# Performance work log

Hardware: AMD Instinct MI355X
Metric: run time of the kernel (lower is better)

## Reference

```python
import jax, jax.numpy as jnp
import numpy as np

EPS = 1e-5


def _conv1x1(h, w, b):
    # 1x1 conv == per-pixel matmul: (b,c,h,w) x (o,c) -> (b,o,h,w)
    return jnp.einsum('bchw,oc->bohw', h, w) + b[None, :, None, None]


def setup_inputs() -> dict:
    key = jax.random.key(0)
    ks = jax.random.split(key, 7)
    B, C, H, W = 4, 512, 64, 64
    s = 0.02
    return {
        'x': jax.random.normal(ks[0], (B, C, H, W), dtype=jnp.float32),
        'wq': jax.random.normal(ks[1], (C, C), dtype=jnp.float32) * s,
        'bq': jax.random.normal(ks[2], (C,), dtype=jnp.float32) * s,
        'wk': jax.random.normal(ks[3], (C, C), dtype=jnp.float32) * s,
        'bk': jax.random.normal(ks[4], (C,), dtype=jnp.float32) * s,
        'wv': jax.random.normal(ks[5], (C, C), dtype=jnp.float32) * s,
        'bv': jax.random.normal(ks[6], (C,), dtype=jnp.float32) * s,
    }


def reference(x, wq, bq, wk, bk, wv, bv):
    B, C, H, W = x.shape
    # InstanceNorm2d (affine=False): normalize over spatial dims per (b, c)
    mu = jnp.mean(x, axis=(2, 3), keepdims=True)
    var = jnp.var(x, axis=(2, 3), keepdims=True)  # biased, matches torch
    h_ = (x - mu) * jax.lax.rsqrt(var + EPS)

    q = _conv1x1(h_, wq, bq).reshape(B, C, H * W)  # (b, c, n)
    k = _conv1x1(h_, wk, bk).reshape(B, C, H * W)
    v = _conv1x1(h_, wv, bv).reshape(B, C, H * W)

    scale = float(int(C)) ** (-0.5)
    attn = jnp.einsum('bcq,bck->bqk', q, k) * scale  # (b, n_q, n_k)
    attn = jax.nn.softmax(attn, axis=-1)
    # torch: bmm(v, attn.permute(0,2,1)) -> A[b,c,q] = sum_k v[b,c,k] * attn[b,q,k]
    A = jnp.einsum('bck,bqk->bcq', v, attn).reshape(B, C, H, W)
    return x + A
```

## Files before the change

### kernel.cpp

```cpp
#include <hip/hip_runtime.h>
#include <hip/hip_bf16.h>
#include <cstdint>

#define B_ 4
#define C_ 512
#define N_ 4096

typedef unsigned short u16;
typedef unsigned char u8;
typedef __bf16 bf16x8 __attribute__((ext_vector_type(8)));
typedef float f32x4 __attribute__((ext_vector_type(4)));

union U16B { uint4 u; bf16x8 v; };

__device__ __forceinline__ bf16x8 ld16g(const u16* p) {
  U16B t; t.u = *(const uint4*)p; return t.v;
}

__device__ __forceinline__ u16 f2bf(float f) {
  uint32_t u = __builtin_bit_cast(uint32_t, f);
  u = (u + 0x7FFFu + ((u >> 16) & 1u)) >> 16;
  return (u16)u;
}
__device__ __forceinline__ float bf2f(u16 h) {
  uint32_t u = ((uint32_t)h) << 16;
  return __builtin_bit_cast(float, u);
}

__device__ __forceinline__ u8 f2fp8(float f) {
  uint32_t u = __builtin_bit_cast(uint32_t, f);
  uint32_t s = (u >> 24) & 0x80u;
  uint32_t a = u & 0x7FFFFFFFu;
  if (a >= 0x43700000u) return (u8)(s | 0x7E);
  if (a < 0x3C800000u) {
    float af = __builtin_bit_cast(float, a);
    int m = (int)(af * 512.0f + 0.5f);
    return (u8)(s | (uint32_t)m);
  }
  uint32_t r = (a + 0x7FFFFu + ((a >> 20) & 1u)) >> 20;
  return (u8)(s | (r - (120u << 3)));
}

typedef const __attribute__((address_space(1))) uint32_t* gas_p;
typedef __attribute__((address_space(3))) uint32_t* las_p;
__device__ __forceinline__ void gld16(const void* g, void* l) {
  __builtin_amdgcn_global_load_lds((gas_p)g, (las_p)l, 16, 0, 0);
}

#define SCEXP 0.06376149809794171f

__global__ __launch_bounds__(256) void cvt_w(const float* __restrict__ w, u16* __restrict__ o) {
  int i = blockIdx.x * 256 + threadIdx.x;
  float4 v = ((const float4*)w)[i];
  ushort4 r;
  r.x = f2bf(v.x); r.y = f2bf(v.y); r.z = f2bf(v.z); r.w = f2bf(v.w);
  ((ushort4*)o)[i] = r;
}

__global__ __launch_bounds__(1024) void pack_bias(const float* __restrict__ bq,
    const float* __restrict__ bk, float* __restrict__ o) {
  int i = threadIdx.x;
  o[i] = (i < 512) ? bq[i] : bk[i - 512];
}

__global__ __launch_bounds__(256) void inorm_stats(const float* __restrict__ x,
    float* __restrict__ mu, float* __restrict__ rstd) {
  int bc = blockIdx.x;
  const float4* p = (const float4*)(x + (size_t)bc * N_);
  float s = 0.f, ss = 0.f;
  for (int i = threadIdx.x; i < N_ / 4; i += 256) {
    float4 v = p[i];
    s  += v.x + v.y + v.z + v.w;
    ss += v.x * v.x + v.y * v.y + v.z * v.z + v.w * v.w;
  }
#pragma unroll
  for (int off = 32; off > 0; off >>= 1) {
    s  += __shfl_down(s, off);
    ss += __shfl_down(ss, off);
  }
  __shared__ float as_[4], ass_[4];
  if ((threadIdx.x & 63) == 0) { as_[threadIdx.x >> 6] = s; ass_[threadIdx.x >> 6] = ss; }
  __syncthreads();
  if (threadIdx.x == 0) {
    float S  = as_[0] + as_[1] + as_[2] + as_[3];
    float SS = ass_[0] + ass_[1] + ass_[2] + ass_[3];
    float m  = S * (1.f / N_);
    float var = SS * (1.f / N_) - m * m;
    mu[bc] = m;
    rstd[bc] = rsqrtf(var + 1e-5f);
  }
}

__global__ __launch_bounds__(256) void norm_transpose(const float* __restrict__ x,
    const float* __restrict__ mu, const float* __restrict__ rstd, u16* __restrict__ hT) {
  __shared__ u16 tile[64][66];
  int b = blockIdx.z, c0 = blockIdx.y * 64, n0 = blockIdx.x * 64;
  int tn = threadIdx.x & 63, t4 = threadIdx.x >> 6;
  const float* xb = x + ((size_t)b * C_ + c0) * N_ + n0;
#pragma unroll
  for (int it = 0; it < 16; ++it) {
    int c = t4 + it * 4;
    float m  = mu[b * C_ + c0 + c];
    float rs = rstd[b * C_ + c0 + c];
    tile[c][tn] = f2bf((xb[(size_t)c * N_ + tn] - m) * rs);
  }
  __syncthreads();
  u16* hTb = hT + ((size_t)b * N_ + n0) * C_ + c0;
#pragma unroll
  for (int it = 0; it < 16; ++it) {
    int n = t4 + it * 4;
    hTb[(size_t)n * C_ + tn] = tile[tn][n];
  }
}

#define EPI_QK8  2
#define EPI_V8   3

template<int EPI>
__global__ __launch_bounds__(256) void gemm128(
    const u16* __restrict__ A, const u16* __restrict__ B,
    const float* __restrict__ aux, void* __restrict__ Out,
    int klen, int lda, int ldb, int ldo,
    long sAz, long sBz, long sOz)
{
  int z = blockIdx.z;
  const u16* Ab = A + (size_t)z * sAz;
  const u16* Bb = B + (size_t)z * sBz;
  int m0 = blockIdx.x * 128, n0 = blockIdx.y * 128;
  int t = threadIdx.x, w = t >> 6, l = t & 63;
  int wr = w >> 1, wc = w & 1;
  int l16 = l & 15, lg = l >> 4;

  __shared__ char smem[65536];

  int srow = t >> 3;
  int scol = ((t & 7) << 4) ^ ((srow & 7) << 4);
  size_t ldaB = (size_t)lda * 2, ldbB = (size_t)ldb * 2;

  f32x4 acc[4][4] = {};
  int nsteps = klen >> 6;

#define STAGE(step, d) {                                                     \
    size_t kbyte = (size_t)(step) * 128 + scol;                              \
    char* lb = smem + (d) * 32768;                                           \
    _Pragma("unroll")                                                        \
    for (int i = 0; i < 4; ++i) {                                            \
      int row = i * 32 + srow;                                               \
      gld16((const char*)Ab + (size_t)(m0 + row) * ldaB + kbyte,             \
            lb + (size_t)(i * 256 + t) * 16);                                \
      gld16((const char*)Bb + (size_t)(n0 + row) * ldbB + kbyte,             \
            lb + 16384 + (size_t)(i * 256 + t) * 16);                        \
    }                                                                        \
  }

  STAGE(0, 0);
  __syncthreads();
  int cur = 0;
  int sw = (l16 & 7) << 4;
  for (int s = 0; s < nsteps; ++s) {
    if (s + 1 < nsteps) STAGE(s + 1, cur ^ 1);
    const char* Al = smem + cur * 32768;
    const char* Bl = Al + 16384;
#pragma unroll
    for (int kc = 0; kc < 2; ++kc) {
      int cb = (kc * 64 + lg * 16) ^ sw;
      bf16x8 af[4], bf[4];
#pragma unroll
      for (int mf = 0; mf < 4; ++mf)
        af[mf] = *(const bf16x8*)(Al + (wr * 64 + mf * 16 + l16) * 128 + cb);
#pragma unroll
      for (int nf = 0; nf < 4; ++nf)
        bf[nf] = *(const bf16x8*)(Bl + (wc * 64 + nf * 16 + l16) * 128 + cb);
#pragma unroll
      for (int mf = 0; mf < 4; ++mf)
#pragma unroll
        for (int nf = 0; nf < 4; ++nf)
          acc[mf][nf] = __builtin_amdgcn_mfma_f32_16x16x32_bf16(af[mf], bf[nf], acc[mf][nf], 0, 0, 0);
    }
    __syncthreads();
    cur ^= 1;
  }
#undef STAGE

  u8* ob = (u8*)Out + (size_t)z * sOz;
  char* sb = smem;
  float bc[4];
  if constexpr (EPI == EPI_QK8) {
#pragma unroll
    for (int nf = 0; nf < 4; ++nf) bc[nf] = aux[n0 + wc * 64 + nf * 16 + l16];
  }
#pragma unroll
  for (int mf = 0; mf < 4; ++mf) {
#pragma unroll
    for (int r = 0; r < 4; ++r) {
      int rowl = wr * 64 + mf * 16 + lg * 4 + r;
      float brow = (EPI == EPI_V8) ? aux[m0 + rowl] : 0.f;
#pragma unroll
      for (int nf = 0; nf < 4; ++nf) {
        int cl = wc * 64 + nf * 16 + l16;
        int w6 = cl & 63;
        int clp = (cl & 64) | (((w6 >> 3) & 3) * 16) | (((w6 >> 5) & 1) * 8) | (w6 & 7);
        float v = acc[mf][nf][r] + (EPI == EPI_QK8 ? bc[nf] : brow);
        sb[rowl * 128 + clp] = (char)f2fp8(v);
      }
    }
  }
  __syncthreads();
#pragma unroll
  for (int it = 0; it < 4; ++it) {
    int idx = it * 256 + t;
    int row = idx >> 3, seg = idx & 7;
    *(uint4*)(ob + (size_t)(m0 + row) * ldo + n0 + seg * 16) =
        *(const uint4*)(sb + row * 128 + seg * 16);
  }
}

__global__ __launch_bounds__(512, 2) void exp8(
    const u8* __restrict__ qk8, float* __restrict__ dsumAll, u8* __restrict__ Pall)
{
  int fid = blockIdx.x;
  int rid = (fid & 7) * 256 + (fid >> 3);
  int z = rid >> 9;
  int r9 = rid & 511;
  int c2 = r9 >> 8;
  int r8 = r9 & 255;
  int sm = r8 >> 6, w6s = r8 & 63;
  int m0 = (c2 * 16 + (sm >> 1) * 8 + (w6s >> 3)) * 128;
  int n0 = ((sm & 1) * 8 + (w6s & 7)) * 256;

  const u8* Ab = qk8 + (size_t)z * ((size_t)N_ * 1024);
  const u8* Bb = Ab + 512;
  float* dsum = dsumAll + (size_t)z * N_;
  u8* Pp = Pall + (size_t)z * (size_t)N_ * N_;

  int t = threadIdx.x, w = t >> 6, l = t & 63;
  int wr = w >> 2, wc = w & 3;
  int l16 = l & 15, lg = l >> 4;

  __shared__ char smem[49152];

  f32x4 acc[4][4] = {};
  int rg = ((lg ^ ((l16 >> 1) & 3)) & 3) << 4;

#define STG8(step, lb) {                                                     \
    size_t kb = (size_t)(step) * 64;                                         \
    {                                                                        \
      int row = t >> 2, g = t & 3;                                           \
      int sg = (g ^ ((row >> 1) & 3)) << 4;                                  \
      gld16((const char*)Ab + (size_t)(m0 + row) * 1024 + kb + sg,           \
            (lb) + (size_t)t * 16);                                          \
    }                                                                        \
    _Pragma("unroll")                                                        \
    for (int i = 0; i < 2; ++i) {                                            \
      int s2 = i * 512 + t;                                                  \
      int row = s2 >> 2, g = s2 & 3;                                         \
      int sg = (g ^ ((row >> 1) & 3)) << 4;                                  \
      gld16((const char*)Bb + (size_t)(n0 + row) * 1024 + kb + sg,           \
            (lb) + 8192 + (size_t)s2 * 16);                                  \
    }                                                                        \
  }

#define COMP8(lb) {                                                          \
    const char* Al = (lb);                                                   \
    const char* Bl = (lb) + 8192;                                            \
    uint4 af[4], bf[4];                                                      \
    _Pragma("unroll")                                                        \
    for (int mf = 0; mf < 4; ++mf)                                           \
      af[mf] = *(const uint4*)(Al + (wr * 64 + mf * 16 + l16) * 64 + rg);    \
    _Pragma("unroll")                                                        \
    for (int nf = 0; nf < 4; ++nf)                                           \
      bf[nf] = *(const uint4*)(Bl + (wc * 64 + nf * 16 + l16) * 64 + rg);    \
    _Pragma("unroll")                                                        \
    for (int kk = 0; kk < 2; ++kk) {                                         \
      _Pragma("unroll")                                                      \
      for (int mf = 0; mf < 4; ++mf) {                                       \
        long long a8 = ((long long)(kk ? af[mf].w : af[mf].y) << 32) |       \
                       (unsigned int)(kk ? af[mf].z : af[mf].x);             \
        _Pragma("unroll")                                                    \
        for (int nf = 0; nf < 4; ++nf) {                                     \
          long long b8 = ((long long)(kk ? bf[nf].w : bf[nf].y) << 32) |     \
                         (unsigned int)(kk ? bf[nf].z : bf[nf].x);           \
          acc[mf][nf] = __builtin_amdgcn_mfma_f32_16x16x32_fp8_fp8(          \
              a8, b8, acc[mf][nf], 0, 0, 0);                                 \
        }                                                                    \
      }                                                                      \
    }                                                                        \
  }

  char* buf0 = smem;
  char* buf1 = smem + 24576;

  STG8(0, buf0);
#pragma unroll
  for (int s = 0; s < 8; ++s) {
    char* cb = (s & 1) ? buf1 : buf0;
    char* nb = (s & 1) ? buf0 : buf1;
    if (s < 7) {
      STG8(s + 1, nb);
      asm volatile("s_waitcnt vmcnt(3)" ::: "memory");
    } else {
      asm volatile("s_waitcnt vmcnt(0)" ::: "memory");
    }
    __builtin_amdgcn_s_barrier();
    __builtin_amdgcn_sched_barrier(0);
    COMP8(cb);
    __builtin_amdgcn_sched_barrier(0);
    __builtin_amdgcn_s_barrier();
  }
#undef STG8
#undef COMP8

#pragma unroll
  for (int mf = 0; mf < 4; ++mf) {
#pragma unroll
    for (int r = 0; r < 4; ++r) {
      int row = wr * 64 + mf * 16 + lg * 4 + r;
      float rs = 0.f;
#pragma unroll
      for (int nf = 0; nf < 4; ++nf) {
        int cl = wc * 64 + nf * 16 + l16;
        int w6 = cl & 63;
        int clp = (cl & 192) | (((w6 >> 3) & 3) * 16) | (((w6 >> 5) & 1) * 8) | (w6 & 7);
        float p = __builtin_amdgcn_exp2f(acc[mf][nf][r] * SCEXP);
        rs += p;
        smem[row * 256 + clp] = (char)f2fp8(p);
      }
      rs += __shfl_xor(rs, 1); rs += __shfl_xor(rs, 2);
      rs += __shfl_xor(rs, 4); rs += __shfl_xor(rs, 8);
      if (l16 == 0) atomicAdd(&dsum[m0 + row], rs);
    }
  }
  __syncthreads();
#pragma unroll
  for (int it = 0; it < 4; ++it) {
    int idx = it * 512 + t;
    int row = idx >> 4, seg = idx & 15;
    *(uint4*)(Pp + ((size_t)(m0 + row) * N_ + n0 + seg * 16)) =
        *(const uint4*)(smem + row * 256 + seg * 16);
  }
}

__global__ __launch_bounds__(256, 4) void pv8(
    const u8* __restrict__ vM8, const u8* __restrict__ P8,
    const float* __restrict__ denom, const float* __restrict__ x,
    float* __restrict__ out)
{
  int fid = blockIdx.x;
  int rid = (fid & 7) * 64 + (fid >> 3);
  int z = rid >> 7;
  int r7 = rid & 127;
  int n0 = (r7 >> 2) * 128;
  int m0 = (r7 & 3) * 128;

  const u8* Ab = vM8 + (size_t)z * ((size_t)C_ * N_);
  const u8* Bb = P8 + (size_t)z * ((size_t)N_ * N_);
  const float* db = denom + (size_t)z * N_;
  const float* xb = x + (size_t)z * ((size_t)C_ * N_);
  float* ob = out + (size_t)z * ((size_t)C_ * N_);

  int t = threadIdx.x, w = t >> 6, l = t & 63;
  int wr = w >> 1, wc = w & 1;
  int l16 = l & 15, lg = l >> 4;

  __shared__ char smem[32768];

  f32x4 acc[4][4] = {};
  int rg = ((lg ^ ((l16 >> 1) & 3)) & 3) << 4;

#define STGP(step, lb) {                                                     \
    size_t kb = (size_t)(step) * 64;                                         \
    _Pragma("unroll")                                                        \
    for (int i = 0; i < 2; ++i) {                                            \
      int s2 = i * 256 + t;                                                  \
      int row = s2 >> 2, g = s2 & 3;                                         \
      int sg = (g ^ ((row >> 1) & 3)) << 4;                                  \
      gld16((const char*)Ab + (size_t)(m0 + row) * N_ + kb + sg,             \
            (lb) + (size_t)s2 * 16);                                         \
      gld16((const char*)Bb + (size_t)(n0 + row) * N_ + kb + sg,             \
            (lb) + 8192 + (size_t)s2 * 16);                                  \
    }                                                                        \
  }

#define COMPP(lb) {                                                          \
    const char* Al = (lb);                                                   \
    const char* Bl = (lb) + 8192;                                            \
    uint4 af[4], bf[4];                                                      \
    _Pragma("unroll")                                                        \
    for (int mf = 0; mf < 4; ++mf)                                           \
      af[mf] = *(const uint4*)(Al + (wr * 64 + mf * 16 + l16) * 64 + rg);    \
    _Pragma("unroll")                                                        \
    for (int nf = 0; nf < 4; ++nf)                                           \
      bf[nf] = *(const uint4*)(Bl + (wc * 64 + nf * 16 + l16) * 64 + rg);    \
    _Pragma("unroll")                                                        \
    for (int kk = 0; kk < 2; ++kk) {                                         \
      _Pragma("unroll")                                                      \
      for (int mf = 0; mf < 4; ++mf) {                                       \
        long long a8 = ((long long)(kk ? af[mf].w : af[mf].y) << 32) |       \
                       (unsigned int)(kk ? af[mf].z : af[mf].x);             \
        _Pragma("unroll")                                                    \
        for (int nf = 0; nf < 4; ++nf) {                                     \
          long long b8 = ((long long)(kk ? bf[nf].w : bf[nf].y) << 32) |     \
                         (unsigned int)(kk ? bf[nf].z : bf[nf].x);           \
          acc[mf][nf] = __builtin_amdgcn_mfma_f32_16x16x32_fp8_fp8(          \
              a8, b8, acc[mf][nf], 0, 0, 0);                                 \
        }                                                                    \
      }                                                                      \
    }                                                                        \
  }

  char* buf0 = smem;
  char* buf1 = smem + 16384;

  STGP(0, buf0);
#pragma unroll 2
  for (int s = 0; s < 64; ++s) {
    char* cb = (s & 1) ? buf1 : buf0;
    char* nb = (s & 1) ? buf0 : buf1;
    if (s < 63) {
      STGP(s + 1, nb);
      asm volatile("s_waitcnt vmcnt(4)" ::: "memory");
    } else {
      asm volatile("s_waitcnt vmcnt(0)" ::: "memory");
    }
    __builtin_amdgcn_s_barrier();
    __builtin_amdgcn_sched_barrier(0);
    COMPP(cb);
    __builtin_amdgcn_sched_barrier(0);
    __builtin_amdgcn_s_barrier();
  }
#undef STGP
#undef COMPP

  float rd[4];
#pragma unroll
  for (int nf = 0; nf < 4; ++nf)
    rd[nf] = 1.0f / db[n0 + wc * 64 + nf * 16 + l16];
#pragma unroll
  for (int mf = 0; mf < 4; ++mf) {
#pragma unroll
    for (int r = 0; r < 4; ++r) {
      int row = m0 + wr * 64 + mf * 16 + lg * 4 + r;
#pragma unroll
      for (int nf = 0; nf < 4; ++nf) {
        int col = n0 + wc * 64 + nf * 16 + l16;
        size_t o = (size_t)row * N_ + col;
        ob[o] = xb[o] + acc[mf][nf][r] * rd[nf];
      }
    }
  }
}

__global__ __launch_bounds__(256) void gemm_abT(
    const u16* __restrict__ A, const u16* __restrict__ Bm,
    const float* __restrict__ bias, u16* __restrict__ out,
    int ldo, int bias_is_row)
{
  int w = threadIdx.x >> 6, l = threadIdx.x & 63;
  int l16 = l & 15, lg = l >> 4;
  int m0 = blockIdx.x * 128 + (w >> 1) * 64;
  int n0 = blockIdx.y * 128 + (w & 1) * 64;
  f32x4 acc[4][4] = {};
  const u16* Ab = A  + (size_t)(m0 + l16) * 512 + lg * 8;
  const u16* Bb = Bm + (size_t)(n0 + l16) * 512 + lg * 8;
  for (int kc = 0; kc < 512; kc += 32) {
    bf16x8 af[4], bf[4];
#pragma unroll
    for (int i = 0; i < 4; ++i) af[i] = ld16g(Ab + (size_t)(i * 16) * 512 + kc);
#pragma unroll
    for (int j = 0; j < 4; ++j) bf[j] = ld16g(Bb + (size_t)(j * 16) * 512 + kc);
#pragma unroll
    for (int i = 0; i < 4; ++i)
#pragma unroll
      for (int j = 0; j < 4; ++j)
        acc[i][j] = __builtin_amdgcn_mfma_f32_16x16x32_bf16(af[i], bf[j], acc[i][j], 0, 0, 0);
  }
#pragma unroll
  for (int i = 0; i < 4; ++i) {
#pragma unroll
    for (int j = 0; j < 4; ++j) {
      int col = n0 + j * 16 + l16;
#pragma unroll
      for (int r = 0; r < 4; ++r) {
        int row = m0 + i * 16 + lg * 4 + r;
        float v = acc[i][j][r] + (bias_is_row ? bias[row] : bias[col]);
        out[(size_t)row * ldo + col] = f2bf(v);
      }
    }
  }
}

#define NQ 32
#define NKB 64
__global__ __launch_bounds__(512) void attn_kernel(
    const u16* __restrict__ qT, const u16* __restrict__ kT, const u16* __restrict__ vM,
    const float* __restrict__ x, float* __restrict__ out)
{
  int b = blockIdx.y;
  int nq0 = blockIdx.x * NQ;
  const u16* qTb = qT + (size_t)b * N_ * C_;
  const u16* kTb = kT + (size_t)b * N_ * C_;
  const u16* vb  = vM + (size_t)b * C_ * N_;
  const float* xb = x + (size_t)b * C_ * N_;
  float* ob = out + (size_t)b * C_ * N_;

  int tid = threadIdx.x;
  int w = tid >> 6, l = tid & 63, l16 = l & 15, lg = l >> 4;
  int nqf = w & 1, nkf = w >> 1;
  int c0 = w * 64;

  __shared__ u16 qlds[32][520];
  __shared__ u16 Plds[32][72];
  __shared__ float dpart[32][16];
  __shared__ float dfin[32];

  for (int idx = tid; idx < 32 * 64; idx += 512) {
    int row = idx >> 6, cg = idx & 63;
    *(uint4*)&qlds[row][cg * 8] = *(const uint4*)(qTb + (size_t)(nq0 + row) * C_ + cg * 8);
  }
  __syncthreads();

  f32x4 acc[2][4] = {};
  float dreg = 0.f;
  int drow = tid >> 4, dcol = (tid & 15) * 4;

  for (int nk0 = 0; nk0 < N_; nk0 += NKB) {
    f32x4 s = {0.f, 0.f, 0.f, 0.f};
    const u16* krow = kTb + (size_t)(nk0 + nkf * 16 + l16) * C_ + lg * 8;
#pragma unroll 4
    for (int kc = 0; kc < 16; ++kc) {
      U16B tq; tq.u = *(const uint4*)&qlds[nqf * 16 + l16][kc * 32 + lg * 8];
      bf16x8 kf = ld16g(krow + kc * 32);
      s = __builtin_amdgcn_mfma_f32_16x16x32_bf16(tq.v, kf, s, 0, 0, 0);
    }
    __syncthreads();
#pragma unroll
    for (int r = 0; r < 4; ++r) {
      float p = __builtin_amdgcn_exp2f(s[r] * SCEXP);
      Plds[nqf * 16 + lg * 4 + r][nkf * 16 + l16] = f2bf(p);
    }
    __syncthreads();
#pragma unroll
    for (int r = 0; r < 4; ++r) dreg += bf2f(Plds[drow][dcol + r]);
#pragma unroll
    for (int kk = 0; kk < 2; ++kk) {
      bf16x8 pf[2];
#pragma unroll
      for (int i = 0; i < 2; ++i) {
        U16B t2; t2.u = *(const uint4*)&Plds[i * 16 + l16][kk * 32 + lg * 8];
        pf[i] = t2.v;
      }
#pragma unroll
      for (int j = 0; j < 4; ++j) {
        bf16x8 vf = ld16g(vb + (size_t)(c0 + j * 16 + l16) * N_ + nk0 + kk * 32 + lg * 8);
#pragma unroll
        for (int i = 0; i < 2; ++i)
          acc[i][j] = __builtin_amdgcn_mfma_f32_16x16x32_bf16(pf[i], vf, acc[i][j], 0, 0, 0);
      }
    }
  }

  dpart[drow][tid & 15] = dreg;
  __syncthreads();
  if (tid < 32) {
    float s2 = 0.f;
#pragma unroll
    for (int g = 0; g < 16; ++g) s2 += dpart[tid][g];
    dfin[tid] = s2;
  }
  __syncthreads();

#pragma unroll
  for (int i = 0; i < 2; ++i) {
    float dinv[4];
#pragma unroll
    for (int r = 0; r < 4; ++r) dinv[r] = 1.f / dfin[i * 16 + lg * 4 + r];
    int nbase = nq0 + i * 16 + lg * 4;
#pragma unroll
    for (int j = 0; j < 4; ++j) {
      int c = c0 + j * 16 + l16;
      float4 xv = *(const float4*)(xb + (size_t)c * N_ + nbase);
      float4 o;
      o.x = xv.x + acc[i][j][0] * dinv[0];
      o.y = xv.y + acc[i][j][1] * dinv[1];
      o.z = xv.z + acc[i][j][2] * dinv[2];
      o.w = xv.w + acc[i][j][3] * dinv[3];
      *(float4*)(ob + (size_t)c * N_ + nbase) = o;
    }
  }
}

extern "C" void kernel_launch(void* const* d_in, const int* in_sizes, int n_in,
                              void* d_out, int out_size, void* d_ws, size_t ws_size,
                              hipStream_t stream) {
  (void)in_sizes; (void)n_in; (void)out_size;
  const float* x  = (const float*)d_in[0];
  const float* wq = (const float*)d_in[1];
  const float* bq = (const float*)d_in[2];
  const float* wk = (const float*)d_in[3];
  const float* bk = (const float*)d_in[4];
  const float* wv = (const float*)d_in[5];
  const float* bv = (const float*)d_in[6];
  float* out = (float*)d_out;
  char* ws = (char*)d_ws;

  const size_t NC = (size_t)N_ * C_;
  const size_t NEED = 136380416;

  if (ws_size >= NEED) {
    u16*   wbf_q = (u16*)(ws);
    u16*   wbf_k = (u16*)(ws + 524288);
    u16*   wbf_v = (u16*)(ws + 1048576);
    float* bqk   = (float*)(ws + 1572864);
    float* mu    = (float*)(ws + 1581056);
    float* rstd  = (float*)(ws + 1589248);
    u16*   hT    = (u16*)(ws + 1597440);
    u8*    qk8   = (u8*)(ws + 18874368);
    u8*    vM8   = (u8*)(ws + 52428800);
    float* denom = (float*)(ws + 69206016);
    u8*    P8    = (u8*)(ws + 69271552);

    cvt_w<<<256, 256, 0, stream>>>(wq, wbf_q);
    cvt_w<<<256, 256, 0, stream>>>(wk, wbf_k);
    cvt_w<<<256, 256, 0, stream>>>(wv, wbf_v);
    pack_bias<<<1, 1024, 0, stream>>>(bq, bk, bqk);
    inorm_stats<<<B_ * C_, 256, 0, stream>>>(x, mu, rstd);
    norm_transpose<<<dim3(N_ / 64, C_ / 64, B_), 256, 0, stream>>>(x, mu, rstd, hT);
    hipMemsetAsync(denom, 0, 4 * N_ * sizeof(float), stream);

    gemm128<EPI_QK8><<<dim3(32, 8, 4), 256, 0, stream>>>(
        hT, wbf_q, bqk, qk8, 512, 512, 512, 1024, (long)NC, 0, (long)N_ * 1024);
    gemm128<EPI_V8><<<dim3(4, 32, 4), 256, 0, stream>>>(
        wbf_v, hT, bv, vM8, 512, 512, 512, 4096, 0, (long)NC, (long)NC);

    exp8<<<2048, 512, 0, stream>>>(qk8, denom, P8);

    pv8<<<512, 256, 0, stream>>>(vM8, P8, denom, x, out);
  } else {
    u16*   wbf_q = (u16*)(ws);
    u16*   wbf_k = (u16*)(ws + 524288);
    u16*   wbf_v = (u16*)(ws + 1048576);
    float* mu    = (float*)(ws + 1572864);
    float* rstd  = (float*)(ws + 1581056);
    u16*   hT    = (u16*)(ws + 1589248);
    u16*   qT    = (u16*)(ws + 18366464);
    u16*   kT    = (u16*)(ws + 35143680);
    u16*   vM    = (u16*)(ws + 51920896);

    cvt_w<<<256, 256, 0, stream>>>(wq, wbf_q);
    cvt_w<<<256, 256, 0, stream>>>(wk, wbf_k);
    cvt_w<<<256, 256, 0, stream>>>(wv, wbf_v);
    inorm_stats<<<B_ * C_, 256, 0, stream>>>(x, mu, rstd);
    norm_transpose<<<dim3(N_ / 64, C_ / 64, B_), 256, 0, stream>>>(x, mu, rstd, hT);

    for (int b = 0; b < B_; ++b) {
      const u16* hTb = hT + (size_t)b * NC;
      u16* qTb = qT + (size_t)b * NC;
      u16* kTb = kT + (size_t)b * NC;
      u16* vMb = vM + (size_t)b * NC;
      gemm_abT<<<dim3(N_ / 128, C_ / 128), 256, 0, stream>>>(hTb, wbf_q, bq, qTb, C_, 0);
      gemm_abT<<<dim3(N_ / 128, C_ / 128), 256, 0, stream>>>(hTb, wbf_k, bk, kTb, C_, 0);
      gemm_abT<<<dim3(C_ / 128, N_ / 128), 256, 0, stream>>>(wbf_v, hTb, bv, vMb, N_, 1);
    }
    attn_kernel<<<dim3(N_ / NQ, B_), 512, 0, stream>>>(qT, kT, vM, x, out);
  }
}
```

Before: 227.7 us.

## Split exp kernel into single-wave 64x64 tiles and store probabilities as bf8

Replaces the 512-thread, 128x256-tile exp kernel with a one-wavefront kernel over 64x64 tiles. It uses a triple-buffered global-to-LDS pipeline with no block barriers and launches 16384 blocks. Probabilities are now encoded as bf8 (e5m2) through a half-precision conversion rather than fp8, and the PV kernel switches to fp8*bf8 MFMA with 8-byte LDS fragment loads. The column permutation in the epilogue stores is dropped. Smaller tiles re-read the Q/K operands more often, and bf8 carries less mantissa precision for the softmax weights.

```diff
diff --git a/kernel.cpp b/kernel.cpp
--- a/kernel.cpp
+++ b/kernel.cpp
@@ -39,6 +39,13 @@
   }
   uint32_t r = (a + 0x7FFFFu + ((a >> 20) & 1u)) >> 20;
   return (u8)(s | (r - (120u << 3)));
+}
+
+__device__ __forceinline__ u8 f2bf8pos(float f) {
+  _Float16 h = (_Float16)f;
+  u16 hb = __builtin_bit_cast(unsigned short, h);
+  hb = (u16)(hb + 0x7Fu + ((hb >> 8) & 1u));
+  return (u8)(hb >> 8);
 }
 
 typedef const __attribute__((address_space(1))) uint32_t* gas_p;
@@ -198,10 +205,8 @@
 #pragma unroll
       for (int nf = 0; nf < 4; ++nf) {
         int cl = wc * 64 + nf * 16 + l16;
-        int w6 = cl & 63;
-        int clp = (cl & 64) | (((w6 >> 3) & 3) * 16) | (((w6 >> 5) & 1) * 8) | (w6 & 7);
         float v = acc[mf][nf][r] + (EPI == EPI_QK8 ? bc[nf] : brow);
-        sb[rowl * 128 + clp] = (char)f2fp8(v);
+        sb[rowl * 128 + cl] = (char)f2fp8(v);
       }
     }
   }
@@ -215,128 +220,106 @@
   }
 }
 
-__global__ __launch_bounds__(512, 2) void exp8(
+__global__ __launch_bounds__(64, 2) void exp_wave(
     const u8* __restrict__ qk8, float* __restrict__ dsumAll, u8* __restrict__ Pall)
 {
   int fid = blockIdx.x;
-  int rid = (fid & 7) * 256 + (fid >> 3);
-  int z = rid >> 9;
-  int r9 = rid & 511;
-  int c2 = r9 >> 8;
-  int r8 = r9 & 255;
-  int sm = r8 >> 6, w6s = r8 & 63;
-  int m0 = (c2 * 16 + (sm >> 1) * 8 + (w6s >> 3)) * 128;
-  int n0 = ((sm & 1) * 8 + (w6s & 7)) * 256;
+  int rid = (fid & 7) * 2048 + (fid >> 3);
+  int z = rid >> 12;
+  int r12 = rid & 4095;
+  int st = r12 >> 6, w6 = r12 & 63;
+  int m0 = ((st >> 3) * 8 + (w6 >> 3)) * 64;
+  int n0 = ((st & 7) * 8 + (w6 & 7)) * 64;
 
   const u8* Ab = qk8 + (size_t)z * ((size_t)N_ * 1024);
   const u8* Bb = Ab + 512;
   float* dsum = dsumAll + (size_t)z * N_;
   u8* Pp = Pall + (size_t)z * (size_t)N_ * N_;
 
-  int t = threadIdx.x, w = t >> 6, l = t & 63;
-  int wr = w >> 2, wc = w & 3;
-  int l16 = l & 15, lg = l >> 4;
-
-  __shared__ char smem[49152];
+  int l = threadIdx.x, l16 = l & 15, lg = l >> 4;
+
+  __shared__ char smem[12288];
 
   f32x4 acc[4][4] = {};
-  int rg = ((lg ^ ((l16 >> 1) & 3)) & 3) << 4;
-
-#define STG8(step, lb) {                                                     \
-    size_t kb = (size_t)(step) * 64;                                         \
-    {                                                                        \
-      int row = t >> 2, g = t & 3;                                           \
-      int sg = (g ^ ((row >> 1) & 3)) << 4;                                  \
-      gld16((const char*)Ab + (size_t)(m0 + row) * 1024 + kb + sg,           \
-            (lb) + (size_t)t * 16);                                          \
+  int ga = ((((lg >> 1) ^ ((l16 >> 2) & 1)) << 4) | ((lg & 1) << 3));
+
+#define STGE(s, lb) {                                                        \
+    size_t kb = (size_t)(s) * 32;                                            \
+    _Pragma("unroll")                                                        \
+    for (int i = 0; i < 2; ++i) {                                            \
+      int slot = i * 64 + l;                                                 \
+      int row = slot >> 1;                                                   \
+      int gs = ((slot & 1) ^ ((row >> 2) & 1)) << 4;                         \
+      gld16((const char*)Ab + (size_t)(m0 + row) * 1024 + kb + gs,           \
+            (lb) + slot * 16);                                               \
+      gld16((const char*)Bb + (size_t)(n0 + row) * 1024 + kb + gs,           \
+            (lb) + 2048 + slot * 16);                                        \
     }                                                                        \
-    _Pragma("unroll")                                                        \
-    for (int i = 0; i < 2; ++i) {                                            \
-      int s2 = i * 512 + t;                                                  \
-      int row = s2 >> 2, g = s2 & 3;                                         \
-      int sg = (g ^ ((row >> 1) & 3)) << 4;                                  \
-      gld16((const char*)Bb + (size_t)(n0 + row) * 1024 + kb + sg,           \
-            (lb) + 8192 + (size_t)s2 * 16);                                  \
-    }                                                                        \
-  }
-
-#define COMP8(lb) {                                                          \
-    const char* Al = (lb);                                                   \
-    const char* Bl = (lb) + 8192;                                            \
-    uint4 af[4], bf[4];                                                      \
+  }
+
+#define COMPE(lb) {                                                          \
+    long long a8[4], b8[4];                                                  \
     _Pragma("unroll")                                                        \
     for (int mf = 0; mf < 4; ++mf)                                           \
-      af[mf] = *(const uint4*)(Al + (wr * 64 + mf * 16 + l16) * 64 + rg);    \
+      a8[mf] = *(const long long*)((lb) + (mf * 16 + l16) * 32 + ga);        \
     _Pragma("unroll")                                                        \
     for (int nf = 0; nf < 4; ++nf)                                           \
-      bf[nf] = *(const uint4*)(Bl + (wc * 64 + nf * 16 + l16) * 64 + rg);    \
-    _Pragma("unroll")                                                        \
-    for (int kk = 0; kk < 2; ++kk) {                                         \
+      b8[nf] = *(const long long*)((lb) + 2048 + (nf * 16 + l16) * 32 + ga); \
+    _Pragma("unroll")                                                        \
+    for (int mf = 0; mf < 4; ++mf)                                           \
       _Pragma("unroll")                                                      \
-      for (int mf = 0; mf < 4; ++mf) {                                       \
-        long long a8 = ((long long)(kk ? af[mf].w : af[mf].y) << 32) |       \
-                       (unsigned int)(kk ? af[mf].z : af[mf].x);             \
-        _Pragma("unroll")                                                    \
-        for (int nf = 0; nf < 4; ++nf) {                                     \
-          long long b8 = ((long long)(kk ? bf[nf].w : bf[nf].y) << 32) |     \
-                         (unsigned int)(kk ? bf[nf].z : bf[nf].x);           \
-          acc[mf][nf] = __builtin_amdgcn_mfma_f32_16x16x32_fp8_fp8(          \
-              a8, b8, acc[mf][nf], 0, 0, 0);                                 \
-        }                                                                    \
-      }                                                                      \
-    }                                                                        \
-  }
-
-  char* buf0 = smem;
-  char* buf1 = smem + 24576;
-
-  STG8(0, buf0);
-#pragma unroll
-  for (int s = 0; s < 8; ++s) {
-    char* cb = (s & 1) ? buf1 : buf0;
-    char* nb = (s & 1) ? buf0 : buf1;
-    if (s < 7) {
-      STG8(s + 1, nb);
-      asm volatile("s_waitcnt vmcnt(3)" ::: "memory");
-    } else {
-      asm volatile("s_waitcnt vmcnt(0)" ::: "memory");
-    }
-    __builtin_amdgcn_s_barrier();
+      for (int nf = 0; nf < 4; ++nf)                                         \
+        acc[mf][nf] = __builtin_amdgcn_mfma_f32_16x16x32_fp8_fp8(            \
+            a8[mf], b8[nf], acc[mf][nf], 0, 0, 0);                           \
+  }
+
+  char* b0 = smem;
+  char* b1 = smem + 4096;
+  char* b2 = smem + 8192;
+
+  STGE(0, b0);
+  STGE(1, b1);
+#pragma unroll
+  for (int s = 0; s < 14; ++s) {
+    STGE(s + 2, b2);
+    asm volatile("s_waitcnt vmcnt(8)" ::: "memory");
     __builtin_amdgcn_sched_barrier(0);
-    COMP8(cb);
-    __builtin_amdgcn_sched_barrier(0);
-    __builtin_amdgcn_s_barrier();
-  }
-#undef STG8
-#undef COMP8
+    COMPE(b0);
+    char* tmp = b0; b0 = b1; b1 = b2; b2 = tmp;
+  }
+  asm volatile("s_waitcnt vmcnt(4)" ::: "memory");
+  __builtin_amdgcn_sched_barrier(0);
+  COMPE(b0);
+  { char* tmp = b0; b0 = b1; b1 = b2; b2 = tmp; }
+  asm volatile("s_waitcnt vmcnt(0)" ::: "memory");
+  __builtin_amdgcn_sched_barrier(0);
+  COMPE(b0);
+#undef STGE
+#undef COMPE
 
 #pragma unroll
   for (int mf = 0; mf < 4; ++mf) {
 #pragma unroll
     for (int r = 0; r < 4; ++r) {
-      int row = wr * 64 + mf * 16 + lg * 4 + r;
+      int row = mf * 16 + lg * 4 + r;
       float rs = 0.f;
 #pragma unroll
       for (int nf = 0; nf < 4; ++nf) {
-        int cl = wc * 64 + nf * 16 + l16;
-        int w6 = cl & 63;
-        int clp = (cl & 192) | (((w6 >> 3) & 3) * 16) | (((w6 >> 5) & 1) * 8) | (w6 & 7);
         float p = __builtin_amdgcn_exp2f(acc[mf][nf][r] * SCEXP);
         rs += p;
-        smem[row * 256 + clp] = (char)f2fp8(p);
+        smem[row * 64 + nf * 16 + l16] = (char)f2bf8pos(p);
       }
       rs += __shfl_xor(rs, 1); rs += __shfl_xor(rs, 2);
       rs += __shfl_xor(rs, 4); rs += __shfl_xor(rs, 8);
       if (l16 == 0) atomicAdd(&dsum[m0 + row], rs);
     }
   }
-  __syncthreads();
 #pragma unroll
   for (int it = 0; it < 4; ++it) {
-    int idx = it * 512 + t;
-    int row = idx >> 4, seg = idx & 15;
-    *(uint4*)(Pp + ((size_t)(m0 + row) * N_ + n0 + seg * 16)) =
-        *(const uint4*)(smem + row * 256 + seg * 16);
+    int slot = it * 64 + l;
+    int row = slot >> 2, g = slot & 3;
+    uint4 v = *(const uint4*)(smem + row * 64 + g * 16);
+    *(uint4*)(Pp + ((size_t)(m0 + row) * N_ + n0 + g * 16)) = v;
   }
 }
 
@@ -365,7 +348,9 @@
   __shared__ char smem[32768];
 
   f32x4 acc[4][4] = {};
-  int rg = ((lg ^ ((l16 >> 1) & 3)) & 3) << 4;
+  int sxr = (l16 >> 1) & 3;
+  int off0 = ((((lg >> 1) + 0) ^ sxr) << 4) | ((lg & 1) << 3);
+  int off1 = ((((lg >> 1) + 2) ^ sxr) << 4) | ((lg & 1) << 3);
 
 #define STGP(step, lb) {                                                     \
     size_t kb = (size_t)(step) * 64;                                         \
@@ -384,28 +369,28 @@
 #define COMPP(lb) {                                                          \
     const char* Al = (lb);                                                   \
     const char* Bl = (lb) + 8192;                                            \
-    uint4 af[4], bf[4];                                                      \
+    long long a0[4], a1[4], c0v[4], c1v[4];                                  \
+    _Pragma("unroll")                                                        \
+    for (int mf = 0; mf < 4; ++mf) {                                         \
+      int ro = (wr * 64 + mf * 16 + l16) * 64;                               \
+      a0[mf] = *(const long long*)(Al + ro + off0);                          \
+      a1[mf] = *(const long long*)(Al + ro + off1);                          \
+    }                                                                        \
+    _Pragma("unroll")                                                        \
+    for (int nf = 0; nf < 4; ++nf) {                                         \
+      int ro = (wc * 64 + nf * 16 + l16) * 64;                               \
+      c0v[nf] = *(const long long*)(Bl + ro + off0);                         \
+      c1v[nf] = *(const long long*)(Bl + ro + off1);                         \
+    }                                                                        \
     _Pragma("unroll")                                                        \
     for (int mf = 0; mf < 4; ++mf)                                           \
-      af[mf] = *(const uint4*)(Al + (wr * 64 + mf * 16 + l16) * 64 + rg);    \
-    _Pragma("unroll")                                                        \
-    for (int nf = 0; nf < 4; ++nf)                                           \
-      bf[nf] = *(const uint4*)(Bl + (wc * 64 + nf * 16 + l16) * 64 + rg);    \
-    _Pragma("unroll")                                                        \
-    for (int kk = 0; kk < 2; ++kk) {                                         \
       _Pragma("unroll")                                                      \
-      for (int mf = 0; mf < 4; ++mf) {                                       \
-        long long a8 = ((long long)(kk ? af[mf].w : af[mf].y) << 32) |       \
-                       (unsigned int)(kk ? af[mf].z : af[mf].x);             \
-        _Pragma("unroll")                                                    \
-        for (int nf = 0; nf < 4; ++nf) {                                     \
-          long long b8 = ((long long)(kk ? bf[nf].w : bf[nf].y) << 32) |     \
-                         (unsigned int)(kk ? bf[nf].z : bf[nf].x);           \
-          acc[mf][nf] = __builtin_amdgcn_mfma_f32_16x16x32_fp8_fp8(          \
-              a8, b8, acc[mf][nf], 0, 0, 0);                                 \
-        }                                                                    \
+      for (int nf = 0; nf < 4; ++nf) {                                       \
+        acc[mf][nf] = __builtin_amdgcn_mfma_f32_16x16x32_fp8_bf8(            \
+            a0[mf], c0v[nf], acc[mf][nf], 0, 0, 0);                          \
+        acc[mf][nf] = __builtin_amdgcn_mfma_f32_16x16x32_fp8_bf8(            \
+            a1[mf], c1v[nf], acc[mf][nf], 0, 0, 0);                          \
       }                                                                      \
-    }                                                                        \
   }
 
   char* buf0 = smem;
@@ -632,7 +617,7 @@
     gemm128<EPI_V8><<<dim3(4, 32, 4), 256, 0, stream>>>(
         wbf_v, hT, bv, vM8, 512, 512, 512, 4096, 0, (long)NC, (long)NC);
 
-    exp8<<<2048, 512, 0, stream>>>(qk8, denom, P8);
+    exp_wave<<<16384, 64, 0, stream>>>(qk8, denom, P8);
 
     pv8<<<512, 256, 0, stream>>>(vM8, P8, denom, x, out);
   } else {
```

New measurement: 287.2 us. +26.1%, slower.

## Pack fp8 epilogue stores with XOR-swizzled LDS, use bf8 for P, raise exp8 occupancy

Applied to the files above, without the earlier changes.

The V8 and exp8 epilogues now pack four fp8 values into one 32-bit LDS store, using an XOR block swizzle in place of the previous per-byte permuted stores. The readback is adjusted to match. The softmax probabilities are now encoded as bf8 (e5m2) through a fast fp16-based conversion, and the PV MFMA changes to fp8×bf8. exp8's launch bound moves to 3 blocks per CU. This cuts epilogue LDS instructions and conversion cost, but lowers P's mantissa precision and adds register pressure from the higher occupancy target.

```diff
diff --git a/kernel.cpp b/kernel.cpp
--- a/kernel.cpp
+++ b/kernel.cpp
@@ -39,6 +39,13 @@
   }
   uint32_t r = (a + 0x7FFFFu + ((a >> 20) & 1u)) >> 20;
   return (u8)(s | (r - (120u << 3)));
+}
+
+__device__ __forceinline__ u8 f2bf8pos(float f) {
+  _Float16 h = (_Float16)f;
+  u16 hb = __builtin_bit_cast(unsigned short, h);
+  hb = (u16)(hb + 0x7Fu + ((hb >> 8) & 1u));
+  return (u8)(hb >> 8);
 }
 
 typedef const __attribute__((address_space(1))) uint32_t* gas_p;
@@ -184,38 +191,60 @@
 
   u8* ob = (u8*)Out + (size_t)z * sOz;
   char* sb = smem;
-  float bc[4];
   if constexpr (EPI == EPI_QK8) {
+    float bc[4];
 #pragma unroll
     for (int nf = 0; nf < 4; ++nf) bc[nf] = aux[n0 + wc * 64 + nf * 16 + l16];
-  }
-#pragma unroll
-  for (int mf = 0; mf < 4; ++mf) {
-#pragma unroll
-    for (int r = 0; r < 4; ++r) {
-      int rowl = wr * 64 + mf * 16 + lg * 4 + r;
-      float brow = (EPI == EPI_V8) ? aux[m0 + rowl] : 0.f;
-#pragma unroll
-      for (int nf = 0; nf < 4; ++nf) {
-        int cl = wc * 64 + nf * 16 + l16;
-        int w6 = cl & 63;
-        int clp = (cl & 64) | (((w6 >> 3) & 3) * 16) | (((w6 >> 5) & 1) * 8) | (w6 & 7);
-        float v = acc[mf][nf][r] + (EPI == EPI_QK8 ? bc[nf] : brow);
-        sb[rowl * 128 + clp] = (char)f2fp8(v);
+#pragma unroll
+    for (int mf = 0; mf < 4; ++mf) {
+#pragma unroll
+      for (int r = 0; r < 4; ++r) {
+        int rowl = wr * 64 + mf * 16 + lg * 4 + r;
+#pragma unroll
+        for (int nf = 0; nf < 4; ++nf) {
+          int cl = wc * 64 + nf * 16 + l16;
+          int w6 = cl & 63;
+          int clp = (cl & 64) | (((w6 >> 3) & 3) * 16) | (((w6 >> 5) & 1) * 8) | (w6 & 7);
+          sb[rowl * 128 + clp] = (char)f2fp8(acc[mf][nf][r] + bc[nf]);
+        }
       }
     }
-  }
-  __syncthreads();
-#pragma unroll
-  for (int it = 0; it < 4; ++it) {
-    int idx = it * 256 + t;
-    int row = idx >> 3, seg = idx & 7;
-    *(uint4*)(ob + (size_t)(m0 + row) * ldo + n0 + seg * 16) =
-        *(const uint4*)(sb + row * 128 + seg * 16);
-  }
-}
-
-__global__ __launch_bounds__(512, 2) void exp8(
+    __syncthreads();
+#pragma unroll
+    for (int it = 0; it < 4; ++it) {
+      int idx = it * 256 + t;
+      int row = idx >> 3, seg = idx & 7;
+      *(uint4*)(ob + (size_t)(m0 + row) * ldo + n0 + seg * 16) =
+          *(const uint4*)(sb + row * 128 + seg * 16);
+    }
+  } else {
+#pragma unroll
+    for (int mf = 0; mf < 4; ++mf) {
+#pragma unroll
+      for (int r = 0; r < 4; ++r) {
+        int rowl = wr * 64 + mf * 16 + lg * 4 + r;
+        float brow = aux[m0 + rowl];
+        uint32_t pk = 0;
+#pragma unroll
+        for (int nf = 0; nf < 4; ++nf)
+          pk |= (uint32_t)f2fp8(acc[mf][nf][r] + brow) << (8 * nf);
+        int blk = (wc ^ ((rowl >> 2) & 1)) << 6;
+        *(uint32_t*)(sb + rowl * 128 + blk + l16 * 4) = pk;
+      }
+    }
+    __syncthreads();
+#pragma unroll
+    for (int it = 0; it < 4; ++it) {
+      int idx = it * 256 + t;
+      int row = idx >> 3, seg = idx & 7;
+      int blk = ((seg >> 2) ^ ((row >> 2) & 1)) << 6;
+      *(uint4*)(ob + (size_t)(m0 + row) * ldo + n0 + seg * 16) =
+          *(const uint4*)(sb + row * 128 + blk + (seg & 3) * 16);
+    }
+  }
+}
+
+__global__ __launch_bounds__(512, 3) void exp8(
     const u8* __restrict__ qk8, float* __restrict__ dsumAll, u8* __restrict__ Pall)
 {
   int fid = blockIdx.x;
@@ -316,15 +345,15 @@
     for (int r = 0; r < 4; ++r) {
       int row = wr * 64 + mf * 16 + lg * 4 + r;
       float rs = 0.f;
+      uint32_t pk = 0;
 #pragma unroll
       for (int nf = 0; nf < 4; ++nf) {
-        int cl = wc * 64 + nf * 16 + l16;
-        int w6 = cl & 63;
-        int clp = (cl & 192) | (((w6 >> 3) & 3) * 16) | (((w6 >> 5) & 1) * 8) | (w6 & 7);
         float p = __builtin_amdgcn_exp2f(acc[mf][nf][r] * SCEXP);
         rs += p;
-        smem[row * 256 + clp] = (char)f2fp8(p);
+        pk |= (uint32_t)f2bf8pos(p) << (8 * nf);
       }
+      int blk = (wc ^ lg) << 6;
+      *(uint32_t*)(smem + row * 256 + blk + l16 * 4) = pk;
       rs += __shfl_xor(rs, 1); rs += __shfl_xor(rs, 2);
       rs += __shfl_xor(rs, 4); rs += __shfl_xor(rs, 8);
       if (l16 == 0) atomicAdd(&dsum[m0 + row], rs);
@@ -335,8 +364,9 @@
   for (int it = 0; it < 4; ++it) {
     int idx = it * 512 + t;
     int row = idx >> 4, seg = idx & 15;
+    int blk = ((seg >> 2) ^ ((row >> 2) & 3)) << 6;
     *(uint4*)(Pp + ((size_t)(m0 + row) * N_ + n0 + seg * 16)) =
-        *(const uint4*)(smem + row * 256 + seg * 16);
+        *(const uint4*)(smem + row * 256 + blk + (seg & 3) * 16);
   }
 }
 
@@ -401,7 +431,7 @@
         for (int nf = 0; nf < 4; ++nf) {                                     \
           long long b8 = ((long long)(kk ? bf[nf].w : bf[nf].y) << 32) |     \
                          (unsigned int)(kk ? bf[nf].z : bf[nf].x);           \
-          acc[mf][nf] = __builtin_amdgcn_mfma_f32_16x16x32_fp8_fp8(          \
+          acc[mf][nf] = __builtin_amdgcn_mfma_f32_16x16x32_fp8_bf8(          \
               a8, b8, acc[mf][nf], 0, 0, 0);                                 \
         }                                                                    \
       }                                                                      \
```

Result: faster. 222.5 us (-2.3%).
